# Kernel optimization log

Measured on AMD Instinct MI355X. Metric: run time of the kernel, lower is better.

Reference implementation:

```python
import jax, jax.numpy as jnp
import numpy as np

EPS = 1e-5

def _layernorm(x, g, b):
    # normalize over last (channel) axis
    mu = jnp.mean(x, axis=-1, keepdims=True)
    var = jnp.var(x, axis=-1, keepdims=True)
    return (x - mu) * jax.lax.rsqrt(var + EPS) * g + b

def _dynamix(xt, wnd, bnd, wnn, bnn):
    # xt: [B, M, N, C]; mixes over the N axis (vectorized form of the per-slice loop)
    B, M, N, C = xt.shape
    d = wnd.shape[1]
    p = xt @ wnd + bnd                       # [B,M,N,d]
    p = p.reshape(B, M, N * d) @ wnn + bnn   # [B,M,N*N]
    p = jax.nn.softmax(p.reshape(B, M, N, N), axis=-1)
    return jnp.einsum('bmij,bmjc->bmic', p, xt)  # [B,M,N,C]

def setup_inputs() -> dict:
    key = jax.random.key(0)
    ks = jax.random.split(key, 10)
    B, C, H, W, d, E = 32, 128, 56, 56, 10, 4
    def n(k, shape, scale=0.02):
        return jax.random.normal(k, shape, jnp.float32) * scale
    return {
        'x': jax.random.normal(ks[0], (B, C, H, W), jnp.float32),
        'ln1_g': jnp.ones((C,), jnp.float32), 'ln1_b': jnp.zeros((C,), jnp.float32),
        'h_wnd': n(ks[1], (C, d)), 'h_bnd': jnp.zeros((d,), jnp.float32),
        'h_wnn': n(ks[2], (W * d, W * W)), 'h_bnn': jnp.zeros((W * W,), jnp.float32),
        'w_wnd': n(ks[3], (C, d)), 'w_bnd': jnp.zeros((d,), jnp.float32),
        'w_wnn': n(ks[4], (H * d, H * H)), 'w_bnn': jnp.zeros((H * H,), jnp.float32),
        'pc_w': n(ks[5], (C, C)), 'pc_b': jnp.zeros((C,), jnp.float32),
        'po_w': n(ks[6], (C, C)), 'po_b': jnp.zeros((C,), jnp.float32),
        'ln2_g': jnp.ones((C,), jnp.float32), 'ln2_b': jnp.zeros((C,), jnp.float32),
        'fc1_w': n(ks[7], (C, E * C)), 'fc1_b': jnp.zeros((E * C,), jnp.float32),
        'fc2_w': n(ks[8], (E * C, C)), 'fc2_b': jnp.zeros((C,), jnp.float32),
    }

def reference(x, ln1_g, ln1_b, h_wnd, h_bnd, h_wnn, h_bnn,
              w_wnd, w_bnd, w_wnn, w_bnn, pc_w, pc_b, po_w, po_b,
              ln2_g, ln2_b, fc1_w, fc1_b, fc2_w, fc2_b):
    # x: [B,C,H,W] -> work channels-last [B,H,W,C]
    xt = jnp.transpose(x, (0, 2, 3, 1))
    # ---- block p1: LN + DynaMixer ----
    u = _layernorm(xt, ln1_g, ln1_b)                 # [B,H,W,C]
    y_h = _dynamix(u, h_wnd, h_bnd, h_wnn, h_bnn)    # mix over W per row
    u_w = jnp.transpose(u, (0, 2, 1, 3))             # [B,W,H,C]
    y_w = _dynamix(u_w, w_wnd, w_bnd, w_wnn, w_bnn)  # mix over H per col
    y_w = jnp.transpose(y_w, (0, 2, 1, 3))           # back to [B,H,W,C]
    y_c = u @ pc_w + pc_b                            # 1x1 conv proj_c
    y = (y_h + y_w + y_c) @ po_w + po_b              # 1x1 conv proj_o
    xt = xt + y                                      # residual (drop_path=0)
    # ---- block p2: LN + MLP ----
    v = _layernorm(xt, ln2_g, ln2_b)
    h = jax.nn.gelu(v @ fc1_w + fc1_b, approximate=False)
    h = h @ fc2_w + fc2_b
    xt = xt + h
    return jnp.transpose(xt, (0, 3, 1, 2))           # [B,C,H,W]
```

## Files before the change

kernel.cpp:

```cpp
#include <hip/hip_runtime.h>
#include <math.h>

#define BB 32
#define CC 128
#define HH 56
#define WW 56
#define HWHW 3136
#define TOK 100352
#define BH 1792
#define NDP 576
#define NNP 3200

typedef __attribute__((ext_vector_type(8))) short bhalf8;
typedef __attribute__((ext_vector_type(4))) float f32x4;
typedef __attribute__((ext_vector_type(4))) unsigned int u32x4;

__device__ inline unsigned short f2bf(float f) {
  unsigned int x = __float_as_uint(f);
  unsigned int r = (x + 0x7FFFu + ((x >> 16) & 1u)) >> 16;
  return (unsigned short)r;
}
__device__ inline float bf2f(unsigned short u) {
  return __uint_as_float(((unsigned int)u) << 16);
}
__device__ inline unsigned int pack2(float a, float b) {
  return (unsigned int)f2bf(a) | ((unsigned int)f2bf(b) << 16);
}
__device__ inline f32x4 MFMA(bhalf8 a, bhalf8 b, f32x4 c) {
  return __builtin_amdgcn_mfma_f32_16x16x32_bf16(a, b, c, 0, 0, 0);
}
template <int CH>
__device__ inline bhalf8 ldsFrag(const unsigned short* base, int row, int chunk) {
  return *reinterpret_cast<const bhalf8*>(base + row * (CH * 8) + ((chunk ^ (row & 7)) * 8));
}
__device__ inline bhalf8 gFrag(const unsigned short* p) {
  return *reinterpret_cast<const bhalf8*>(p);
}
__device__ inline float gelu_f(float x) {
  float x3 = x * x * x;
  float z = 0.7978845608028654f * (x + 0.044715f * x3);
  float e = __expf(2.0f * z);
  float t = 1.0f - 2.0f / (e + 1.0f);
  return 0.5f * x * (1.0f + t);
}

__global__ __launch_bounds__(256) void wtrans_kernel(
    const float* __restrict__ hwnn, const float* __restrict__ wwnn,
    const float* __restrict__ pcw, const float* __restrict__ pow_,
    const float* __restrict__ fc1w, const float* __restrict__ fc2w,
    const float* __restrict__ hwnd, const float* __restrict__ wwnd,
    unsigned short* __restrict__ wnnTh, unsigned short* __restrict__ wnnTw,
    unsigned short* __restrict__ pcT, unsigned short* __restrict__ poT,
    unsigned short* __restrict__ fc1T, unsigned short* __restrict__ fc2T,
    unsigned short* __restrict__ wcatT, u32x4* __restrict__ pdzero) {
  __shared__ unsigned short t[64][65];
  int bid = blockIdx.x;
  int tid = threadIdx.x;
  if (bid >= 940) {
    int gt = (bid - 940) * 256 + tid, gs = 64 * 256;
    for (int i = gt; i < 258048; i += gs) { u32x4 z = {0, 0, 0, 0}; pdzero[i] = z; }
    for (int i = gt; i < 128 * 32; i += gs) {
      int k = i >> 5, n = i & 31;
      float v = n < 10 ? hwnd[k * 10 + n] : (n < 20 ? wwnd[k * 10 + (n - 10)] : 0.f);
      wcatT[n * 128 + k] = f2bf(v);
    }
    return;
  }
  const float* src; unsigned short* dst;
  int K, N, Kp, Np, bx, by;
  if (bid < 450)      { src = hwnn; dst = wnnTh; K = 560; N = 3136; Kp = 576; Np = 3200; int b = bid;       bx = b % 50; by = b / 50; }
  else if (bid < 900) { src = wwnn; dst = wnnTw; K = 560; N = 3136; Kp = 576; Np = 3200; int b = bid - 450; bx = b % 50; by = b / 50; }
  else if (bid < 904) { src = pcw;  dst = pcT;   K = 128; N = 128;  Kp = 128; Np = 128;  int b = bid - 900; bx = b % 2;  by = b / 2; }
  else if (bid < 908) { src = pow_; dst = poT;   K = 128; N = 128;  Kp = 128; Np = 128;  int b = bid - 904; bx = b % 2;  by = b / 2; }
  else if (bid < 924) { src = fc1w; dst = fc1T;  K = 128; N = 512;  Kp = 128; Np = 512;  int b = bid - 908; bx = b % 8;  by = b / 8; }
  else                { src = fc2w; dst = fc2T;  K = 512; N = 128;  Kp = 512; Np = 128;  int b = bid - 924; bx = b % 2;  by = b / 2; }
  int n0 = bx * 64, k0 = by * 64;
  for (int idx = tid; idx < 4096; idx += 256) {
    int kk = idx >> 6, nn = idx & 63;
    float v = (k0 + kk < K && n0 + nn < N) ? src[(size_t)(k0 + kk) * N + n0 + nn] : 0.f;
    t[nn][kk] = f2bf(v);
  }
  __syncthreads();
  for (int idx = tid; idx < 4096; idx += 256) {
    int nn = idx >> 6, kk = idx & 63;
    if (n0 + nn < Np && k0 + kk < Kp)
      dst[(size_t)(n0 + nn) * Kp + k0 + kk] = t[nn][kk];
  }
}

__global__ __launch_bounds__(256) void ln1_kernel(const float* __restrict__ x,
    const float* __restrict__ g, const float* __restrict__ bt,
    unsigned short* __restrict__ ubf, unsigned short* __restrict__ xcl) {
  int bh = blockIdx.x;
  int b = bh / HH, h = bh % HH;
  __shared__ float lds[WW][CC + 1];
  __shared__ float mu[WW], rs[WW];
  const float* xp = x + ((size_t)b * CC) * HWHW + (size_t)h * WW;
  for (int idx = threadIdx.x; idx < CC * WW; idx += 256) {
    int c = idx / WW, w = idx % WW;
    lds[w][c] = xp[(size_t)c * HWHW + w];
  }
  __syncthreads();
  if (threadIdx.x < WW) {
    int w = threadIdx.x;
    float s = 0.f, ss = 0.f;
    for (int c = 0; c < CC; ++c) { float v = lds[w][c]; s += v; ss += v * v; }
    float m = s * (1.0f / CC);
    float var = ss * (1.0f / CC) - m * m;
    mu[w] = m; rs[w] = rsqrtf(var + 1e-5f);
  }
  __syncthreads();
  unsigned short* up = ubf + (size_t)bh * (WW * CC);
  unsigned short* xc = xcl + (size_t)bh * (WW * CC);
  for (int idx = threadIdx.x; idx < WW * CC; idx += 256) {
    int w = idx >> 7, c = idx & 127;
    float v = lds[w][c];
    up[idx] = f2bf((v - mu[w]) * rs[w] * g[c] + bt[c]);
    xc[idx] = f2bf(v);
  }
}

__global__ __launch_bounds__(256) void pd_mfma(const unsigned short* __restrict__ ubf,
    const unsigned short* __restrict__ wcatT, const float* __restrict__ hbnd,
    const float* __restrict__ wbnd, unsigned short* __restrict__ pdh,
    unsigned short* __restrict__ pdw) {
  __shared__ __align__(16) unsigned short sU[64 * 128];
  __shared__ __align__(16) unsigned short sW[32 * 128];
  int tid = threadIdx.x;
  int tok0 = blockIdx.x * 64;
  #pragma unroll
  for (int i = 0; i < 4; ++i) {
    int s = i * 256 + tid; int r = s >> 4, c = s & 15;
    u32x4 v = *reinterpret_cast<const u32x4*>(ubf + (size_t)(tok0 + r) * 128 + c * 8);
    *reinterpret_cast<u32x4*>(sU + r * 128 + ((c ^ (r & 7)) * 8)) = v;
  }
  #pragma unroll
  for (int i = 0; i < 2; ++i) {
    int s = i * 256 + tid; int r = s >> 4, c = s & 15;
    u32x4 v = *reinterpret_cast<const u32x4*>(wcatT + (size_t)r * 128 + c * 8);
    *reinterpret_cast<u32x4*>(sW + r * 128 + ((c ^ (r & 7)) * 8)) = v;
  }
  __syncthreads();
  int wid = tid >> 6, lane = tid & 63, l16 = lane & 15, lk = lane >> 4;
  f32x4 acc[2] = {};
  #pragma unroll
  for (int kk = 0; kk < 4; ++kk) {
    bhalf8 a = ldsFrag<16>(sU, wid * 16 + l16, kk * 4 + lk);
    #pragma unroll
    for (int f = 0; f < 2; ++f) {
      bhalf8 b = ldsFrag<16>(sW, f * 16 + l16, kk * 4 + lk);
      acc[f] = MFMA(a, b, acc[f]);
    }
  }
  #pragma unroll
  for (int f = 0; f < 2; ++f) {
    int n = f * 16 + l16;
    #pragma unroll
    for (int r = 0; r < 4; ++r) {
      int tok = tok0 + wid * 16 + lk * 4 + r;
      float v = acc[f][r];
      if (n < 10) {
        pdh[((size_t)(tok / 56)) * NDP + (size_t)(tok % 56) * 10 + n] = f2bf(v + hbnd[n]);
      } else if (n < 20) {
        int b = tok / HWHW; int rem = tok % HWHW; int hh = rem / 56; int w = rem % 56;
        pdw[((size_t)(b * 56 + w)) * NDP + (size_t)hh * 10 + (n - 10)] = f2bf(v + wbnd[n - 10]);
      }
    }
  }
}

__global__ __launch_bounds__(256) void gemm_logits(
    const unsigned short* __restrict__ pdh, const unsigned short* __restrict__ pdw,
    const unsigned short* __restrict__ wnnTh, const unsigned short* __restrict__ wnnTw,
    const float* __restrict__ hbnn, const float* __restrict__ wbnn,
    unsigned short* __restrict__ ph, unsigned short* __restrict__ pwb) {
  __shared__ __align__(16) unsigned short sA[128 * 64];
  __shared__ __align__(16) unsigned short sB[128 * 64];
  int tid = threadIdx.x;
  int byr = blockIdx.y;
  const unsigned short* A; const unsigned short* BT; const float* bias; unsigned short* Cout;
  int row0;
  if (byr < 14) { A = pdh; BT = wnnTh; bias = hbnn; Cout = ph;  row0 = byr * 128; }
  else          { A = pdw; BT = wnnTw; bias = wbnn; Cout = pwb; row0 = (byr - 14) * 128; }
  int col0 = blockIdx.x * 128;
  int wid = tid >> 6, lane = tid & 63;
  int wm = wid >> 1, wn = wid & 1;
  int l16 = lane & 15, lk = lane >> 4;
  f32x4 acc[4][4] = {};
  for (int k0 = 0; k0 < NDP; k0 += 64) {
    #pragma unroll
    for (int i = 0; i < 4; ++i) {
      int s = i * 256 + tid; int r = s >> 3, c = s & 7;
      u32x4 v = *reinterpret_cast<const u32x4*>(A + (size_t)(row0 + r) * NDP + k0 + c * 8);
      *reinterpret_cast<u32x4*>(sA + r * 64 + ((c ^ (r & 7)) * 8)) = v;
    }
    #pragma unroll
    for (int i = 0; i < 4; ++i) {
      int s = i * 256 + tid; int r = s >> 3, c = s & 7;
      u32x4 v = *reinterpret_cast<const u32x4*>(BT + (size_t)(col0 + r) * NDP + k0 + c * 8);
      *reinterpret_cast<u32x4*>(sB + r * 64 + ((c ^ (r & 7)) * 8)) = v;
    }
    __syncthreads();
    bhalf8 af[4][2], bf[4][2];
    #pragma unroll
    for (int f = 0; f < 4; ++f)
      #pragma unroll
      for (int kk = 0; kk < 2; ++kk) {
        af[f][kk] = ldsFrag<8>(sA, wm * 64 + f * 16 + l16, kk * 4 + lk);
        bf[f][kk] = ldsFrag<8>(sB, wn * 64 + f * 16 + l16, kk * 4 + lk);
      }
    #pragma unroll
    for (int i = 0; i < 4; ++i)
      #pragma unroll
      for (int j = 0; j < 4; ++j) {
        acc[i][j] = MFMA(af[i][0], bf[j][0], acc[i][j]);
        acc[i][j] = MFMA(af[i][1], bf[j][1], acc[i][j]);
      }
    __syncthreads();
  }
  #pragma unroll
  for (int i = 0; i < 4; ++i) {
    int rbase = row0 + wm * 64 + i * 16 + lk * 4;
    #pragma unroll
    for (int j = 0; j < 4; ++j) {
      int col = col0 + wn * 64 + j * 16 + l16;
      if (col < HWHW) {
        float bv = bias[col];
        #pragma unroll
        for (int r = 0; r < 4; ++r)
          Cout[(size_t)(rbase + r) * NNP + col] = f2bf(acc[i][j][r] + bv);
      }
    }
  }
}

__global__ __launch_bounds__(256) void softmax56_kernel(unsigned short* __restrict__ ph,
                                                        unsigned short* __restrict__ pw) {
  int wave = (blockIdx.x * 256 + threadIdx.x) >> 6;
  int lane = threadIdx.x & 63;
  if (wave >= 2 * TOK) return;
  unsigned short* buf = wave < TOK ? ph : pw;
  int row = wave < TOK ? wave : wave - TOK;
  int bh = row / 56, i = row % 56;
  unsigned short* p = buf + (size_t)bh * NNP + (size_t)i * 56;
  float xv = lane < WW ? bf2f(p[lane]) : -INFINITY;
  float m = xv;
  for (int o = 32; o > 0; o >>= 1) m = fmaxf(m, __shfl_xor(m, o));
  float e = lane < WW ? __expf(xv - m) : 0.f;
  float s = e;
  for (int o = 32; o > 0; o >>= 1) s += __shfl_xor(s, o);
  if (lane < WW) p[lane] = f2bf(e / s);
}

__global__ __launch_bounds__(256) void mixh_pc(const unsigned short* __restrict__ ph,
    const unsigned short* __restrict__ ubf, const unsigned short* __restrict__ pcT,
    const float* __restrict__ pcb, unsigned short* __restrict__ accm) {
  int bh = blockIdx.x;
  int tok0 = bh * 56;
  __shared__ __align__(16) unsigned short sUt[128 * 64];
  int tid = threadIdx.x;
  for (int s = tid; s < 1024; s += 256) {
    int j = s >> 4, cc = s & 15;
    unsigned short e8[8] = {0, 0, 0, 0, 0, 0, 0, 0};
    if (j < 56)
      *reinterpret_cast<u32x4*>(e8) =
          *reinterpret_cast<const u32x4*>(ubf + (size_t)(tok0 + j) * 128 + cc * 8);
    #pragma unroll
    for (int e = 0; e < 8; ++e) {
      int cf = cc * 8 + e;
      sUt[cf * 64 + (((j >> 3) ^ (cf & 7)) * 8) + (j & 7)] = e8[e];
    }
  }
  __syncthreads();
  int lane = tid & 63, l16 = lane & 15, lk = lane >> 4, wn = tid >> 6;
  const unsigned short* prow = ph + (size_t)bh * NNP;
  f32x4 acc[4][2] = {};
  #pragma unroll
  for (int kk = 0; kk < 2; ++kk) {
    bhalf8 a[4], b[2];
    #pragma unroll
    for (int i = 0; i < 4; ++i)
      a[i] = gFrag(prow + (i * 16 + l16) * 56 + (kk * 4 + lk) * 8);
    #pragma unroll
    for (int j = 0; j < 2; ++j) b[j] = ldsFrag<8>(sUt, wn * 32 + j * 16 + l16, kk * 4 + lk);
    #pragma unroll
    for (int i = 0; i < 4; ++i)
      #pragma unroll
      for (int j = 0; j < 2; ++j) acc[i][j] = MFMA(a[i], b[j], acc[i][j]);
  }
  #pragma unroll
  for (int kk = 0; kk < 4; ++kk) {
    bhalf8 a[4], b[2];
    #pragma unroll
    for (int i = 0; i < 4; ++i)
      a[i] = gFrag(ubf + (size_t)(tok0 + i * 16 + l16) * 128 + (kk * 4 + lk) * 8);
    #pragma unroll
    for (int j = 0; j < 2; ++j)
      b[j] = gFrag(pcT + (size_t)(wn * 32 + j * 16 + l16) * 128 + (kk * 4 + lk) * 8);
    #pragma unroll
    for (int i = 0; i < 4; ++i)
      #pragma unroll
      for (int j = 0; j < 2; ++j) acc[i][j] = MFMA(a[i], b[j], acc[i][j]);
  }
  #pragma unroll
  for (int i = 0; i < 4; ++i) {
    int tok = i * 16 + lk * 4;
    #pragma unroll
    for (int j = 0; j < 2; ++j) {
      int c = wn * 32 + j * 16 + l16;
      float bv = pcb[c];
      #pragma unroll
      for (int r = 0; r < 4; ++r)
        if (tok + r < 56)
          accm[(size_t)(tok0 + tok + r) * 128 + c] = f2bf(acc[i][j][r] + bv);
    }
  }
}

__global__ __launch_bounds__(256) void mixw_fin(const unsigned short* __restrict__ pw,
    const unsigned short* __restrict__ ubf, const unsigned short* __restrict__ poT,
    const float* __restrict__ pob, const unsigned short* __restrict__ xcl,
    unsigned short* __restrict__ accXt,
    const float* __restrict__ ln2g, const float* __restrict__ ln2b,
    unsigned short* __restrict__ vbf) {
  int bw = blockIdx.x;
  int bq = bw / 56, w = bw % 56;
  __shared__ __align__(16) unsigned short sUt[128 * 64];
  __shared__ __align__(16) unsigned short sS[64 * 128];
  int tid = threadIdx.x;
  for (int s = tid; s < 1024; s += 256) {
    int j = s >> 4, cc = s & 15;
    unsigned short e8[8] = {0, 0, 0, 0, 0, 0, 0, 0};
    if (j < 56)
      *reinterpret_cast<u32x4*>(e8) =
          *reinterpret_cast<const u32x4*>(ubf + ((size_t)bq * HWHW + (size_t)j * 56 + w) * 128 + cc * 8);
    #pragma unroll
    for (int e = 0; e < 8; ++e) {
      int cf = cc * 8 + e;
      sUt[cf * 64 + (((j >> 3) ^ (cf & 7)) * 8) + (j & 7)] = e8[e];
    }
  }
  for (int s = tid; s < 1024; s += 256) {
    int r = s >> 4, c = s & 15;
    u32x4 v = {0, 0, 0, 0};
    if (r < 56) v = *reinterpret_cast<const u32x4*>(accXt + ((size_t)bq * HWHW + (size_t)r * 56 + w) * 128 + c * 8);
    *reinterpret_cast<u32x4*>(sS + r * 128 + ((c ^ (r & 7)) * 8)) = v;
  }
  __syncthreads();
  int lane = tid & 63, l16 = lane & 15, lk = lane >> 4, wn = tid >> 6;
  const unsigned short* prow = pw + (size_t)bw * NNP;
  f32x4 acc1[4][2] = {};
  #pragma unroll
  for (int kk = 0; kk < 2; ++kk) {
    bhalf8 a[4], b[2];
    #pragma unroll
    for (int i = 0; i < 4; ++i)
      a[i] = gFrag(prow + (i * 16 + l16) * 56 + (kk * 4 + lk) * 8);
    #pragma unroll
    for (int j = 0; j < 2; ++j) b[j] = ldsFrag<8>(sUt, wn * 32 + j * 16 + l16, kk * 4 + lk);
    #pragma unroll
    for (int i = 0; i < 4; ++i)
      #pragma unroll
      for (int j = 0; j < 2; ++j) acc1[i][j] = MFMA(a[i], b[j], acc1[i][j]);
  }
  __syncthreads();
  #pragma unroll
  for (int i = 0; i < 4; ++i) {
    #pragma unroll
    for (int j = 0; j < 2; ++j) {
      int col = wn * 32 + j * 16 + l16;
      #pragma unroll
      for (int r = 0; r < 4; ++r) {
        int row = i * 16 + lk * 4 + r;
        int ad = row * 128 + (((col >> 3) ^ (row & 7)) * 8) + (col & 7);
        sS[ad] = f2bf(bf2f(sS[ad]) + acc1[i][j][r]);
      }
    }
  }
  __syncthreads();
  f32x4 acc2[4][2] = {};
  #pragma unroll
  for (int kk = 0; kk < 4; ++kk) {
    bhalf8 a[4], b[2];
    #pragma unroll
    for (int i = 0; i < 4; ++i) a[i] = ldsFrag<16>(sS, i * 16 + l16, kk * 4 + lk);
    #pragma unroll
    for (int j = 0; j < 2; ++j)
      b[j] = gFrag(poT + (size_t)(wn * 32 + j * 16 + l16) * 128 + (kk * 4 + lk) * 8);
    #pragma unroll
    for (int i = 0; i < 4; ++i)
      #pragma unroll
      for (int j = 0; j < 2; ++j) acc2[i][j] = MFMA(a[i], b[j], acc2[i][j]);
  }
  __syncthreads();
  #pragma unroll
  for (int i = 0; i < 4; ++i) {
    #pragma unroll
    for (int j = 0; j < 2; ++j) {
      int c = wn * 32 + j * 16 + l16;
      float bv = pob[c];
      #pragma unroll
      for (int r = 0; r < 4; ++r) {
        int row = i * 16 + lk * 4 + r;
        if (row < 56) {
          size_t t = (size_t)bq * HWHW + (size_t)row * 56 + w;
          float z = acc2[i][j][r] + bv + bf2f(xcl[t * 128 + c]);
          unsigned short zb = f2bf(z);
          accXt[t * 128 + c] = zb;
          sS[row * 128 + (((c >> 3) ^ (row & 7)) * 8) + (c & 7)] = zb;
        }
      }
    }
  }
  __syncthreads();
  {
    int wid4 = tid >> 6;
    int c0 = 2 * lane;
    float g0 = ln2g[c0], g1 = ln2g[c0 + 1];
    float b0 = ln2b[c0], b1 = ln2b[c0 + 1];
    for (int row = wid4; row < 56; row += 4) {
      int ad = row * 128 + (((c0 >> 3) ^ (row & 7)) * 8) + (c0 & 7);
      unsigned int wrd = *reinterpret_cast<const unsigned int*>(sS + ad);
      float z0 = bf2f((unsigned short)(wrd & 0xFFFFu));
      float z1 = bf2f((unsigned short)(wrd >> 16));
      float s1 = z0 + z1, s2 = z0 * z0 + z1 * z1;
      for (int o = 32; o > 0; o >>= 1) { s1 += __shfl_xor(s1, o); s2 += __shfl_xor(s2, o); }
      float m = s1 * (1.0f / CC);
      float var = s2 * (1.0f / CC) - m * m;
      float rv = rsqrtf(var + 1e-5f);
      float n0 = (z0 - m) * rv * g0 + b0;
      float n1 = (z1 - m) * rv * g1 + b1;
      size_t t = (size_t)bq * HWHW + (size_t)row * 56 + w;
      *reinterpret_cast<unsigned int*>(vbf + t * 128 + c0) = pack2(n0, n1);
    }
  }
}

__global__ __launch_bounds__(256) void gemm_fc1(const unsigned short* __restrict__ vbf,
    const unsigned short* __restrict__ fc1T, const float* __restrict__ b1,
    unsigned short* __restrict__ hbuf) {
  int n = blockIdx.x;
  int sw = (n & 7) * 392 + (n >> 3);
  int hidT = (sw & 3) * 128;
  int tok0 = (sw >> 2) * 128;
  int tid = threadIdx.x;
  int wid = tid >> 6, lane = tid & 63;
  int wm = wid >> 1, wn = wid & 1;
  int l16 = lane & 15, lk = lane >> 4;
  f32x4 acc[4][4] = {};
  #pragma unroll
  for (int kk = 0; kk < 4; ++kk) {
    bhalf8 a[4], b[4];
    #pragma unroll
    for (int i = 0; i < 4; ++i)
      a[i] = gFrag(fc1T + (size_t)(hidT + wm * 64 + i * 16 + l16) * 128 + (kk * 4 + lk) * 8);
    #pragma unroll
    for (int j = 0; j < 4; ++j)
      b[j] = gFrag(vbf + (size_t)(tok0 + wn * 64 + j * 16 + l16) * 128 + (kk * 4 + lk) * 8);
    #pragma unroll
    for (int i = 0; i < 4; ++i)
      #pragma unroll
      for (int j = 0; j < 4; ++j)
        acc[i][j] = MFMA(a[i], b[j], acc[i][j]);
  }
  #pragma unroll
  for (int i = 0; i < 4; ++i) {
    int hidL = wm * 64 + i * 16 + lk * 4;
    f32x4 bv = *reinterpret_cast<const f32x4*>(b1 + hidT + hidL);
    #pragma unroll
    for (int j = 0; j < 4; ++j) {
      int tokL = wn * 64 + j * 16 + l16;
      float v0 = gelu_f(acc[i][j][0] + bv[0]);
      float v1 = gelu_f(acc[i][j][1] + bv[1]);
      float v2 = gelu_f(acc[i][j][2] + bv[2]);
      float v3 = gelu_f(acc[i][j][3] + bv[3]);
      unsigned long long pk = (unsigned long long)pack2(v0, v1)
                            | ((unsigned long long)pack2(v2, v3) << 32);
      *reinterpret_cast<unsigned long long*>(
          hbuf + (size_t)(tok0 + tokL) * 512 + hidT + hidL) = pk;
    }
  }
}

__global__ __launch_bounds__(256) void gemm_fc2(const unsigned short* __restrict__ hbuf,
    const unsigned short* __restrict__ fc2T, const float* __restrict__ b2,
    const unsigned short* __restrict__ xt2, float* __restrict__ out) {
  __shared__ __align__(16) unsigned short xtile[128 * 128];
  __shared__ float b2s[128];
  int tid = threadIdx.x;
  int tok0 = blockIdx.x * 128;
  if (tid < 128) b2s[tid] = b2[tid];
  #pragma unroll
  for (int i = 0; i < 8; ++i) {
    int s = i * 256 + tid; int r = s >> 4, c = s & 15;
    u32x4 v = *reinterpret_cast<const u32x4*>(xt2 + (size_t)(tok0 + r) * 128 + c * 8);
    *reinterpret_cast<u32x4*>(xtile + r * 128 + c * 8) = v;
  }
  __syncthreads();
  int wid = tid >> 6, lane = tid & 63;
  int wm = wid >> 1, wn = wid & 1;
  int l16 = lane & 15, lk = lane >> 4;
  f32x4 acc[4][4] = {};
  #pragma unroll 4
  for (int ck = 0; ck < 16; ++ck) {
    bhalf8 a[4], b[4];
    #pragma unroll
    for (int i = 0; i < 4; ++i)
      a[i] = gFrag(hbuf + (size_t)(tok0 + wm * 64 + i * 16 + l16) * 512 + (ck * 4 + lk) * 8);
    #pragma unroll
    for (int j = 0; j < 4; ++j)
      b[j] = gFrag(fc2T + (size_t)(wn * 64 + j * 16 + l16) * 512 + (ck * 4 + lk) * 8);
    #pragma unroll
    for (int i = 0; i < 4; ++i)
      #pragma unroll
      for (int j = 0; j < 4; ++j)
        acc[i][j] = MFMA(a[i], b[j], acc[i][j]);
  }
  #pragma unroll
  for (int i = 0; i < 4; ++i) {
    int tokL = wm * 64 + i * 16 + lk * 4;
    int tokG = tok0 + tokL;
    int bqv = tokG / HWHW;
    int pos = tokG - bqv * HWHW;
    #pragma unroll
    for (int j = 0; j < 4; ++j) {
      int cL = wn * 64 + j * 16 + l16;
      float bv = b2s[cL];
      f32x4 o;
      #pragma unroll
      for (int r = 0; r < 4; ++r)
        o[r] = acc[i][j][r] + bv + bf2f(xtile[(tokL + r) * 128 + cL]);
      *reinterpret_cast<f32x4*>(out + ((size_t)(bqv * CC + cL)) * HWHW + pos) = o;
    }
  }
}

extern "C" void kernel_launch(void* const* d_in, const int* in_sizes, int n_in,
                              void* d_out, int out_size, void* d_ws, size_t ws_size,
                              hipStream_t stream) {
  const float* x     = (const float*)d_in[0];
  const float* ln1_g = (const float*)d_in[1];
  const float* ln1_b = (const float*)d_in[2];
  const float* h_wnd = (const float*)d_in[3];
  const float* h_bnd = (const float*)d_in[4];
  const float* h_wnn = (const float*)d_in[5];
  const float* h_bnn = (const float*)d_in[6];
  const float* w_wnd = (const float*)d_in[7];
  const float* w_bnd = (const float*)d_in[8];
  const float* w_wnn = (const float*)d_in[9];
  const float* w_bnn = (const float*)d_in[10];
  const float* pc_w  = (const float*)d_in[11];
  const float* pc_b  = (const float*)d_in[12];
  const float* po_w  = (const float*)d_in[13];
  const float* po_b  = (const float*)d_in[14];
  const float* ln2_g = (const float*)d_in[15];
  const float* ln2_b = (const float*)d_in[16];
  const float* fc1_w = (const float*)d_in[17];
  const float* fc1_b = (const float*)d_in[18];
  const float* fc2_w = (const float*)d_in[19];
  const float* fc2_b = (const float*)d_in[20];
  float* out = (float*)d_out;
  char* ws = (char*)d_ws;

  unsigned short* ubf   = (unsigned short*)(ws + 0);
  unsigned short* xcl   = (unsigned short*)(ws + 25690112);
  unsigned short* accXt = (unsigned short*)(ws + 51380224);
  unsigned short* pdh   = (unsigned short*)(ws + 77070336);
  unsigned short* pdw   = (unsigned short*)(ws + 79134720);
  unsigned short* ph    = (unsigned short*)(ws + 81199104);
  unsigned short* pw    = (unsigned short*)(ws + 92667904);
  unsigned short* wnnTh = (unsigned short*)(ws + 104136704);
  unsigned short* wnnTw = (unsigned short*)(ws + 107823104);
  unsigned short* hbuf  = (unsigned short*)(ws + 77070336);
  unsigned short* pcT   = (unsigned short*)(ws + 179830784);
  unsigned short* poT   = (unsigned short*)(ws + 179863552);
  unsigned short* fc1T  = (unsigned short*)(ws + 179896320);
  unsigned short* fc2T  = (unsigned short*)(ws + 180027392);
  unsigned short* wcatT = (unsigned short*)(ws + 180158464);
  unsigned short* vbf   = ubf;

  wtrans_kernel<<<1004, 256, 0, stream>>>(h_wnn, w_wnn, pc_w, po_w, fc1_w, fc2_w,
      h_wnd, w_wnd, wnnTh, wnnTw, pcT, poT, fc1T, fc2T, wcatT, (u32x4*)pdh);
  ln1_kernel<<<BH, 256, 0, stream>>>(x, ln1_g, ln1_b, ubf, xcl);
  pd_mfma<<<TOK / 64, 256, 0, stream>>>(ubf, wcatT, h_bnd, w_bnd, pdh, pdw);
  gemm_logits<<<dim3(NNP / 128, 28), 256, 0, stream>>>(pdh, pdw, wnnTh, wnnTw,
      h_bnn, w_bnn, ph, pw);
  softmax56_kernel<<<(2 * TOK) / 4, 256, 0, stream>>>(ph, pw);
  mixh_pc<<<BH, 256, 0, stream>>>(ph, ubf, pcT, pc_b, accXt);
  mixw_fin<<<BB * WW, 256, 0, stream>>>(pw, ubf, poT, po_b, xcl, accXt,
      ln2_g, ln2_b, vbf);
  gemm_fc1<<<3136, 256, 0, stream>>>(vbf, fc1T, fc1_b, hbuf);
  gemm_fc2<<<TOK / 128, 256, 0, stream>>>(hbuf, fc2T, fc2_b, accXt, out);
}
```

Baseline: 335.7 us.

## Fuse fc1+GELU and fc2 into one kernel keeping hidden activations in LDS

```diff
diff --git a/kernel.cpp b/kernel.cpp
--- a/kernel.cpp
+++ b/kernel.cpp
@@ -436,100 +436,94 @@
   }
 }
 
-__global__ __launch_bounds__(256) void gemm_fc1(const unsigned short* __restrict__ vbf,
+__global__ __launch_bounds__(256) void mlp_fused(const unsigned short* __restrict__ vbf,
     const unsigned short* __restrict__ fc1T, const float* __restrict__ b1,
-    unsigned short* __restrict__ hbuf) {
-  int n = blockIdx.x;
-  int sw = (n & 7) * 392 + (n >> 3);
-  int hidT = (sw & 3) * 128;
-  int tok0 = (sw >> 2) * 128;
-  int tid = threadIdx.x;
-  int wid = tid >> 6, lane = tid & 63;
-  int wm = wid >> 1, wn = wid & 1;
-  int l16 = lane & 15, lk = lane >> 4;
-  f32x4 acc[4][4] = {};
-  #pragma unroll
-  for (int kk = 0; kk < 4; ++kk) {
-    bhalf8 a[4], b[4];
-    #pragma unroll
-    for (int i = 0; i < 4; ++i)
-      a[i] = gFrag(fc1T + (size_t)(hidT + wm * 64 + i * 16 + l16) * 128 + (kk * 4 + lk) * 8);
-    #pragma unroll
-    for (int j = 0; j < 4; ++j)
-      b[j] = gFrag(vbf + (size_t)(tok0 + wn * 64 + j * 16 + l16) * 128 + (kk * 4 + lk) * 8);
-    #pragma unroll
-    for (int i = 0; i < 4; ++i)
-      #pragma unroll
-      for (int j = 0; j < 4; ++j)
-        acc[i][j] = MFMA(a[i], b[j], acc[i][j]);
-  }
-  #pragma unroll
-  for (int i = 0; i < 4; ++i) {
-    int hidL = wm * 64 + i * 16 + lk * 4;
-    f32x4 bv = *reinterpret_cast<const f32x4*>(b1 + hidT + hidL);
-    #pragma unroll
-    for (int j = 0; j < 4; ++j) {
-      int tokL = wn * 64 + j * 16 + l16;
-      float v0 = gelu_f(acc[i][j][0] + bv[0]);
-      float v1 = gelu_f(acc[i][j][1] + bv[1]);
-      float v2 = gelu_f(acc[i][j][2] + bv[2]);
-      float v3 = gelu_f(acc[i][j][3] + bv[3]);
-      unsigned long long pk = (unsigned long long)pack2(v0, v1)
-                            | ((unsigned long long)pack2(v2, v3) << 32);
-      *reinterpret_cast<unsigned long long*>(
-          hbuf + (size_t)(tok0 + tokL) * 512 + hidT + hidL) = pk;
-    }
-  }
-}
-
-__global__ __launch_bounds__(256) void gemm_fc2(const unsigned short* __restrict__ hbuf,
     const unsigned short* __restrict__ fc2T, const float* __restrict__ b2,
     const unsigned short* __restrict__ xt2, float* __restrict__ out) {
-  __shared__ __align__(16) unsigned short xtile[128 * 128];
-  __shared__ float b2s[128];
+  __shared__ __align__(16) unsigned short sH[64 * 512];
+  __shared__ __align__(16) unsigned short xtile[64 * 128];
   int tid = threadIdx.x;
-  int tok0 = blockIdx.x * 128;
-  if (tid < 128) b2s[tid] = b2[tid];
-  #pragma unroll
-  for (int i = 0; i < 8; ++i) {
+  int tok0 = blockIdx.x * 64;
+  int wid = tid >> 6, lane = tid & 63;
+  int l16 = lane & 15, lk = lane >> 4;
+  #pragma unroll
+  for (int i = 0; i < 4; ++i) {
     int s = i * 256 + tid; int r = s >> 4, c = s & 15;
     u32x4 v = *reinterpret_cast<const u32x4*>(xt2 + (size_t)(tok0 + r) * 128 + c * 8);
     *reinterpret_cast<u32x4*>(xtile + r * 128 + c * 8) = v;
   }
-  __syncthreads();
-  int wid = tid >> 6, lane = tid & 63;
+  {
+    int hb = wid * 128;
+    f32x4 acc1[8][4] = {};
+    #pragma unroll
+    for (int kk = 0; kk < 4; ++kk) {
+      bhalf8 a[8], b[4];
+      #pragma unroll
+      for (int i = 0; i < 8; ++i)
+        a[i] = gFrag(fc1T + (size_t)(hb + i * 16 + l16) * 128 + (kk * 4 + lk) * 8);
+      #pragma unroll
+      for (int j = 0; j < 4; ++j)
+        b[j] = gFrag(vbf + (size_t)(tok0 + j * 16 + l16) * 128 + (kk * 4 + lk) * 8);
+      #pragma unroll
+      for (int i = 0; i < 8; ++i)
+        #pragma unroll
+        for (int j = 0; j < 4; ++j)
+          acc1[i][j] = MFMA(a[i], b[j], acc1[i][j]);
+    }
+    #pragma unroll
+    for (int i = 0; i < 8; ++i) {
+      int h0 = hb + i * 16 + lk * 4;
+      f32x4 bv = *reinterpret_cast<const f32x4*>(b1 + h0);
+      int ch = h0 >> 3, hrem = h0 & 7;
+      #pragma unroll
+      for (int j = 0; j < 4; ++j) {
+        int tok = j * 16 + l16;
+        float v0 = gelu_f(acc1[i][j][0] + bv[0]);
+        float v1 = gelu_f(acc1[i][j][1] + bv[1]);
+        float v2 = gelu_f(acc1[i][j][2] + bv[2]);
+        float v3 = gelu_f(acc1[i][j][3] + bv[3]);
+        unsigned long long pk = (unsigned long long)pack2(v0, v1)
+                              | ((unsigned long long)pack2(v2, v3) << 32);
+        *reinterpret_cast<unsigned long long*>(
+            sH + tok * 512 + ((ch ^ (tok & 7)) * 8) + hrem) = pk;
+      }
+    }
+  }
+  __syncthreads();
   int wm = wid >> 1, wn = wid & 1;
-  int l16 = lane & 15, lk = lane >> 4;
-  f32x4 acc[4][4] = {};
+  f32x4 acc2[2][4] = {};
   #pragma unroll 4
   for (int ck = 0; ck < 16; ++ck) {
-    bhalf8 a[4], b[4];
-    #pragma unroll
-    for (int i = 0; i < 4; ++i)
-      a[i] = gFrag(hbuf + (size_t)(tok0 + wm * 64 + i * 16 + l16) * 512 + (ck * 4 + lk) * 8);
+    bhalf8 a[2], b[4];
+    #pragma unroll
+    for (int ii = 0; ii < 2; ++ii) {
+      int row = wm * 32 + ii * 16 + l16;
+      a[ii] = *reinterpret_cast<const bhalf8*>(
+          sH + row * 512 + (((ck * 4 + lk) ^ (row & 7)) * 8));
+    }
     #pragma unroll
     for (int j = 0; j < 4; ++j)
       b[j] = gFrag(fc2T + (size_t)(wn * 64 + j * 16 + l16) * 512 + (ck * 4 + lk) * 8);
     #pragma unroll
-    for (int i = 0; i < 4; ++i)
+    for (int ii = 0; ii < 2; ++ii)
       #pragma unroll
       for (int j = 0; j < 4; ++j)
-        acc[i][j] = MFMA(a[i], b[j], acc[i][j]);
-  }
-  #pragma unroll
-  for (int i = 0; i < 4; ++i) {
-    int tokL = wm * 64 + i * 16 + lk * 4;
+        acc2[ii][j] = MFMA(a[ii], b[j], acc2[ii][j]);
+  }
+  #pragma unroll
+  for (int ii = 0; ii < 2; ++ii) {
+    int tokL = wm * 32 + ii * 16 + lk * 4;
     int tokG = tok0 + tokL;
     int bqv = tokG / HWHW;
     int pos = tokG - bqv * HWHW;
     #pragma unroll
     for (int j = 0; j < 4; ++j) {
       int cL = wn * 64 + j * 16 + l16;
-      float bv = b2s[cL];
+      float bv = b2[cL];
       f32x4 o;
       #pragma unroll
       for (int r = 0; r < 4; ++r)
-        o[r] = acc[i][j][r] + bv + bf2f(xtile[(tokL + r) * 128 + cL]);
+        o[r] = acc2[ii][j][r] + bv + bf2f(xtile[(tokL + r) * 128 + cL]);
       *reinterpret_cast<f32x4*>(out + ((size_t)(bqv * CC + cL)) * HWHW + pos) = o;
     }
   }
@@ -571,12 +565,11 @@
   unsigned short* pw    = (unsigned short*)(ws + 92667904);
   unsigned short* wnnTh = (unsigned short*)(ws + 104136704);
   unsigned short* wnnTw = (unsigned short*)(ws + 107823104);
-  unsigned short* hbuf  = (unsigned short*)(ws + 77070336);
-  unsigned short* pcT   = (unsigned short*)(ws + 179830784);
-  unsigned short* poT   = (unsigned short*)(ws + 179863552);
-  unsigned short* fc1T  = (unsigned short*)(ws + 179896320);
-  unsigned short* fc2T  = (unsigned short*)(ws + 180027392);
-  unsigned short* wcatT = (unsigned short*)(ws + 180158464);
+  unsigned short* pcT   = (unsigned short*)(ws + 111509504);
+  unsigned short* poT   = (unsigned short*)(ws + 111542272);
+  unsigned short* fc1T  = (unsigned short*)(ws + 111575040);
+  unsigned short* fc2T  = (unsigned short*)(ws + 111706112);
+  unsigned short* wcatT = (unsigned short*)(ws + 111837184);
   unsigned short* vbf   = ubf;
 
   wtrans_kernel<<<1004, 256, 0, stream>>>(h_wnn, w_wnn, pc_w, po_w, fc1_w, fc2_w,
@@ -589,6 +582,5 @@
   mixh_pc<<<BH, 256, 0, stream>>>(ph, ubf, pcT, pc_b, accXt);
   mixw_fin<<<BB * WW, 256, 0, stream>>>(pw, ubf, poT, po_b, xcl, accXt,
       ln2_g, ln2_b, vbf);
-  gemm_fc1<<<3136, 256, 0, stream>>>(vbf, fc1T, fc1_b, hbuf);
-  gemm_fc2<<<TOK / 128, 256, 0, stream>>>(hbuf, fc2T, fc2_b, accXt, out);
-}
+  mlp_fused<<<TOK / 64, 256, 0, stream>>>(vbf, fc1T, fc1_b, fc2T, fc2_b, accXt, out);
+}
```

Result: slower. 349.1 us (+4.0%).
